# Kernel tuning notes

Measured on AMD Instinct MI355X. Metric: run time of the kernel, lower is better.

The kernel has to match this reference:

```python
import jax, jax.numpy as jnp
import numpy as np

V, D, L, H, S, B = 32000, 512, 4, 8, 2048, 2
HD = D // H
FF = 4 * D
EPS = 1e-5


def _ln(x, w, b):
    m = jnp.mean(x, axis=-1, keepdims=True)
    v = jnp.var(x, axis=-1, keepdims=True)
    return (x - m) / jnp.sqrt(v + EPS) * w + b


def setup_inputs() -> dict:
    key = jax.random.key(0)
    ks = jax.random.split(key, 32)
    rn = lambda k, shape, s=0.02: jax.random.normal(k, shape, jnp.float32) * s
    return {
        'x': jax.random.randint(ks[0], (B, S), 0, V),
        'tok_emb': rn(ks[1], (V, D)),
        'pos_emb': rn(ks[2], (S, D)),
        'qw': rn(ks[3], (L, D, D)), 'qb': rn(ks[4], (L, D)),
        'kw': rn(ks[5], (L, D, D)), 'kb': rn(ks[6], (L, D)),
        'vw': rn(ks[7], (L, D, D)), 'vb': rn(ks[8], (L, D)),
        'ow': rn(ks[9], (L, D, D)), 'ob': rn(ks[10], (L, D)),
        'qphase': rn(ks[11], (L, H), 0.1),
        'sp_phase': rn(ks[12], (L, D), 0.1),
        'n1w': jnp.ones((L, D), jnp.float32), 'n1b': jnp.zeros((L, D), jnp.float32),
        'n2w': jnp.ones((L, D), jnp.float32), 'n2b': jnp.zeros((L, D), jnp.float32),
        'f1w': rn(ks[13], (L, D, FF)), 'f1b': rn(ks[14], (L, FF)),
        'f2w': rn(ks[15], (L, FF, D)), 'f2b': rn(ks[16], (L, D)),
        'iw': rn(ks[17], (L, D, D)), 'ib': rn(ks[18], (L, D)),
        'gw': rn(ks[19], (L, D, D)), 'gb': rn(ks[20], (L, D)),
        'nw': jnp.ones((D,), jnp.float32), 'nb': jnp.zeros((D,), jnp.float32),
        'outw': rn(ks[21], (D, V)), 'outb': rn(ks[22], (V,)),
    }


def _forward(x, tok_emb, pos_emb, qw, qb, kw, kb, vw, vb, ow, ob, qphase, sp_phase,
             n1w, n1b, n2w, n2b, f1w, f1b, f2w, f2b, iw, ib, gw, gb, nw, nb, outw, outb):
    Bx, Sx = x.shape
    h = tok_emb[x] + pos_emb[:Sx][None, :, :]          # [B,S,D]
    mask = jnp.tril(jnp.ones((Sx, Sx), dtype=bool))    # causal
    scale = 1.0 / np.sqrt(HD).astype(np.float32)
    for l in range(L):
        # quantum attention with phase-modulated scores
        hn = _ln(h, n1w[l], n1b[l])
        q = (hn @ qw[l] + qb[l]).reshape(Bx, Sx, H, HD)
        k = (hn @ kw[l] + kb[l]).reshape(Bx, Sx, H, HD)
        v = (hn @ vw[l] + vb[l]).reshape(Bx, Sx, H, HD)
        scores = jnp.einsum('bqhd,bkhd->bhqk', q, k) * scale
        qi = jnp.cos(qphase[l][None, :, None, None] * scores)
        scores = scores * (1.0 + 0.1 * qi)
        scores = jnp.where(mask[None, None], scores, -jnp.inf)
        attn = jax.nn.softmax(scores, axis=-1)
        o = jnp.einsum('bhqk,bkhd->bqhd', attn, v).reshape(Bx, Sx, D)
        h = h + o @ ow[l] + ob[l]
        # superposition: x * cos(phase * x)
        h = h * jnp.cos(sp_phase[l] * h)
        # feed-forward (exact GELU, as torch default)
        hn2 = _ln(h, n2w[l], n2b[l])
        h = h + jax.nn.gelu(hn2 @ f1w[l] + f1b[l], approximate=False) @ f2w[l] + f2b[l]
        # interference gate
        g = jax.nn.sigmoid(h @ gw[l] + gb[l])
        h = (h @ iw[l] + ib[l]) * g + h * (1.0 - g)
    h = _ln(h, nw, nb)
    return h @ outw + outb                              # [B,S,V] logits


def reference(x, tok_emb, pos_emb, qw, qb, kw, kb, vw, vb, ow, ob, qphase, sp_phase,
              n1w, n1b, n2w, n2b, f1w, f1b, f2w, f2b, iw, ib, gw, gb, nw, nb, outw, outb):
    return _forward(x, tok_emb, pos_emb, qw, qb, kw, kb, vw, vb, ow, ob, qphase, sp_phase,
                    n1w, n1b, n2w, n2b, f1w, f1b, f2w, f2b, iw, ib, gw, gb, nw, nb, outw, outb)
```

## Files before the change

kernel.cpp:

```cpp
#include <hip/hip_runtime.h>
#include <math.h>

#define DIM 512
#define NH 8
#define HD 64
#define SEQ 2048
#define BATCH 2
#define NLAYER 4
#define FFD 2048
#define VOCAB 32000
#define ROWS (BATCH*SEQ)
#define QKV_LD 1536

typedef unsigned short u16;
typedef __attribute__((ext_vector_type(8))) short bfrag;
typedef __attribute__((ext_vector_type(4))) short sfrag4;
typedef __attribute__((ext_vector_type(4))) float facc;

__device__ __forceinline__ u16 f2bf(float f){
  unsigned u = __builtin_bit_cast(unsigned, f);
  u += 0x7fff + ((u>>16)&1);
  return (u16)(u>>16);
}

typedef __attribute__((address_space(3))) unsigned int lds_u32;
typedef const __attribute__((address_space(1))) unsigned int glob_u32;
__device__ __forceinline__ void gload16(const void* g, void* l){
  __builtin_amdgcn_global_load_lds((glob_u32*)g, (lds_u32*)l, 16, 0, 0);
}

template<int N> __device__ __forceinline__ void wait_vmcnt(){
  if constexpr (N==0)      asm volatile("s_waitcnt vmcnt(0)" ::: "memory");
  else if constexpr (N==3) asm volatile("s_waitcnt vmcnt(3)" ::: "memory");
  else if constexpr (N==4) asm volatile("s_waitcnt vmcnt(4)" ::: "memory");
  else if constexpr (N==6) asm volatile("s_waitcnt vmcnt(6)" ::: "memory");
  else if constexpr (N==8) asm volatile("s_waitcnt vmcnt(8)" ::: "memory");
  else static_assert(N==0, "unsupported vmcnt");
}

__global__ void transpose_w(const float* __restrict__ in, u16* __restrict__ out,
                            int K, int N, size_t zStride, int nOff, int imode){
  __shared__ float t[32][33];
  const int bz = blockIdx.z;
  const float* I = in + (size_t)bz*K*N;
  u16* O = out + (size_t)bz*zStride;
  const int n0 = blockIdx.x*32, k0 = blockIdx.y*32;
  #pragma unroll
  for (int i=0;i<4;i++){
    int k = k0 + threadIdx.y + 8*i;
    t[threadIdx.y+8*i][threadIdx.x] = I[(size_t)k*N + n0 + threadIdx.x];
  }
  __syncthreads();
  #pragma unroll
  for (int i=0;i<4;i++){
    int n = n0 + threadIdx.y + 8*i;
    int np = (imode==0) ? n : ((n>>4)*32 + (n&15) + (imode==2 ? 16 : 0));
    O[(size_t)(nOff+np)*K + k0 + threadIdx.x] = f2bf(t[threadIdx.x][threadIdx.y+8*i]);
  }
}

__global__ void concat3_k(const float* __restrict__ a, const float* __restrict__ b,
                          const float* __restrict__ c, float* __restrict__ o){
  int idx = blockIdx.x*256 + threadIdx.x;
  int l = idx/1536, r = idx%1536;
  float v = (r<512) ? a[l*512+r] : (r<1024 ? b[l*512+r-512] : c[l*512+r-1024]);
  o[idx] = v;
}
__global__ void concat2i_k(const float* __restrict__ ib, const float* __restrict__ gb,
                           float* __restrict__ o){
  int idx = blockIdx.x*256 + threadIdx.x;
  int l = idx>>10, cp = idx&1023;
  int bb = cp>>4, c = (bb>>1)*16 + (cp&15);
  o[idx] = (bb&1) ? gb[l*512+c] : ib[l*512+c];
}

__global__ void embed_k(const int* __restrict__ x, const float* __restrict__ tok,
                        const float* __restrict__ pos, float* __restrict__ h){
  int idx = blockIdx.x*256 + threadIdx.x;
  int row = idx >> 7;
  int d4  = idx & 127;
  int s   = row & (SEQ-1);
  int tkn = x[row];
  float4 tv = *(const float4*)(tok + (size_t)tkn*DIM + d4*4);
  float4 pv = *(const float4*)(pos + (size_t)s*DIM + d4*4);
  float4 r; r.x=tv.x+pv.x; r.y=tv.y+pv.y; r.z=tv.z+pv.z; r.w=tv.w+pv.w;
  *(float4*)(h + (size_t)row*DIM + d4*4) = r;
}

__global__ __launch_bounds__(256) void ln_k(const float* __restrict__ h,
    const float* __restrict__ w, const float* __restrict__ bsc,
    u16* __restrict__ out){
  const int wid = threadIdx.x>>6, lane = threadIdx.x&63;
  const int row = blockIdx.x*4 + wid;
  const float* r = h + (size_t)row*DIM + lane*8;
  float4 v0 = *(const float4*)r;
  float4 v1 = *(const float4*)(r+4);
  float s  = v0.x+v0.y+v0.z+v0.w + v1.x+v1.y+v1.z+v1.w;
  float ss = v0.x*v0.x+v0.y*v0.y+v0.z*v0.z+v0.w*v0.w
           + v1.x*v1.x+v1.y*v1.y+v1.z*v1.z+v1.w*v1.w;
  #pragma unroll
  for (int m=1;m<64;m<<=1){ s += __shfl_xor(s,m); ss += __shfl_xor(ss,m); }
  const float mean = s*(1.f/DIM);
  const float var  = ss*(1.f/DIM) - mean*mean;
  const float rsd  = rsqrtf(var + 1e-5f);
  float4 w0 = *(const float4*)(w + lane*8);
  float4 w1 = *(const float4*)(w + lane*8 + 4);
  float4 b0 = *(const float4*)(bsc + lane*8);
  float4 b1 = *(const float4*)(bsc + lane*8 + 4);
  bfrag pk;
  pk[0]=(short)f2bf((v0.x-mean)*rsd*w0.x+b0.x);
  pk[1]=(short)f2bf((v0.y-mean)*rsd*w0.y+b0.y);
  pk[2]=(short)f2bf((v0.z-mean)*rsd*w0.z+b0.z);
  pk[3]=(short)f2bf((v0.w-mean)*rsd*w0.w+b0.w);
  pk[4]=(short)f2bf((v1.x-mean)*rsd*w1.x+b1.x);
  pk[5]=(short)f2bf((v1.y-mean)*rsd*w1.y+b1.y);
  pk[6]=(short)f2bf((v1.z-mean)*rsd*w1.z+b1.z);
  pk[7]=(short)f2bf((v1.w-mean)*rsd*w1.w+b1.w);
  *(bfrag*)&out[(size_t)row*DIM + lane*8] = pk;
}

template<int BM,int BN,int BK,int WRN,int WCN,int DEPTH,int MODE>
__global__ __launch_bounds__(WRN*WCN*64, 2) void gemm_p(
    const u16* __restrict__ A, const u16* __restrict__ BT,
    const float* __restrict__ bias, const float* __restrict__ aux,
    float* __restrict__ Cf, u16* __restrict__ Cb, u16* __restrict__ vt,
    int M, int N, int K){
  constexpr int NTH = WRN*WCN*64;
  constexpr int FI  = BM/(16*WRN);
  constexpr int FJ  = BN/(16*WCN);
  constexpr int CPR = BK/8;
  constexpr int LA  = BM*CPR/NTH;
  constexpr int LB  = BN*CPR/NTH;
  constexpr int LPT = LA+LB;
  constexpr int NKK = BK/32;
  extern __shared__ __align__(16) u16 smem[];
  u16* lds_a = smem;
  u16* lds_b = smem + DEPTH*BM*BK;

  const int tid = threadIdx.x;
  const int wid = tid>>6, lane = tid&63;
  const int wr = wid / WCN, wc = wid % WCN;
  const int lr = lane&15, lg = lane>>4;
  const unsigned nwg = gridDim.x*gridDim.y;
  const unsigned lin = blockIdx.y*gridDim.x + blockIdx.x;
  const unsigned q = nwg >> 3;
  const unsigned sw = (lin & 7)*q + (lin >> 3);
  const int tm = sw % gridDim.x, tn = sw / gridDim.x;

  auto swzf = [](int row)->int{ return (BK==64) ? (row&7) : ((row>>1)&3); };

  auto stage = [&](int t, int buf){
    const int k0 = t*BK;
    #pragma unroll
    for (int i=0;i<LA;i++){
      int u = i*NTH + tid;
      int row = u/CPR, c = (u%CPR) ^ swzf(row);
      gload16(&A[(size_t)(tm*BM+row)*K + k0 + c*8], &lds_a[buf*BM*BK + u*8]);
    }
    #pragma unroll
    for (int i=0;i<LB;i++){
      int u = i*NTH + tid;
      int row = u/CPR, c = (u%CPR) ^ swzf(row);
      gload16(&BT[(size_t)(tn*BN+row)*K + k0 + c*8], &lds_b[buf*BN*BK + u*8]);
    }
  };

  facc acc[FI][FJ] = {};
  const int NT = K/BK;
  stage(0,0);
  if (NT>1) stage(1,1);
  if constexpr (DEPTH==3) { if (NT>2) stage(2,2); }
  for (int t=0;t<NT;t++){
    const int buf = t % DEPTH;
    const u16* la = &lds_a[buf*BM*BK];
    const u16* lb = &lds_b[buf*BN*BK];
    const int rem = NT-1-t;
    if constexpr (DEPTH==3){
      if (rem >= 2) wait_vmcnt<2*LPT>();
      else if (rem == 1) wait_vmcnt<LPT>();
      else wait_vmcnt<0>();
    } else {
      if (rem >= 1) wait_vmcnt<LPT>(); else wait_vmcnt<0>();
    }
    __builtin_amdgcn_s_barrier();
    __builtin_amdgcn_sched_barrier(0);
    bfrag af[FI], bf[FJ];
    #pragma unroll
    for (int i=0;i<FI;i++){
      int row = wr*(FI*16) + i*16 + lr;
      af[i] = *(const bfrag*)&la[row*BK + ((lg ^ swzf(row))*8)];
    }
    #pragma unroll
    for (int j=0;j<FJ;j++){
      int row = wc*(FJ*16) + j*16 + lr;
      bf[j] = *(const bfrag*)&lb[row*BK + ((lg ^ swzf(row))*8)];
    }
    if constexpr (NKK==1){
      asm volatile("s_waitcnt lgkmcnt(0)" ::: "memory");
      __builtin_amdgcn_sched_barrier(0);
      __builtin_amdgcn_s_barrier();
      __builtin_amdgcn_sched_barrier(0);
      if (t+DEPTH<NT) stage(t+DEPTH, buf);
      __builtin_amdgcn_s_setprio(1);
      #pragma unroll
      for (int i=0;i<FI;i++)
        #pragma unroll
        for (int j=0;j<FJ;j++)
          acc[i][j] = __builtin_amdgcn_mfma_f32_16x16x32_bf16(af[i], bf[j], acc[i][j],0,0,0);
      __builtin_amdgcn_s_setprio(0);
    } else {
      __builtin_amdgcn_s_setprio(1);
      #pragma unroll
      for (int i=0;i<FI;i++)
        #pragma unroll
        for (int j=0;j<FJ;j++)
          acc[i][j] = __builtin_amdgcn_mfma_f32_16x16x32_bf16(af[i], bf[j], acc[i][j],0,0,0);
      __builtin_amdgcn_s_setprio(0);
      bfrag af1[FI], bf1[FJ];
      #pragma unroll
      for (int i=0;i<FI;i++){
        int row = wr*(FI*16) + i*16 + lr;
        af1[i] = *(const bfrag*)&la[row*BK + (((4+lg) ^ swzf(row))*8)];
      }
      #pragma unroll
      for (int j=0;j<FJ;j++){
        int row = wc*(FJ*16) + j*16 + lr;
        bf1[j] = *(const bfrag*)&lb[row*BK + (((4+lg) ^ swzf(row))*8)];
      }
      asm volatile("s_waitcnt lgkmcnt(0)" ::: "memory");
      __builtin_amdgcn_sched_barrier(0);
      __builtin_amdgcn_s_barrier();
      __builtin_amdgcn_sched_barrier(0);
      if (t+DEPTH<NT) stage(t+DEPTH, buf);
      __builtin_amdgcn_s_setprio(1);
      #pragma unroll
      for (int i=0;i<FI;i++)
        #pragma unroll
        for (int j=0;j<FJ;j++)
          acc[i][j] = __builtin_amdgcn_mfma_f32_16x16x32_bf16(af1[i], bf1[j], acc[i][j],0,0,0);
      __builtin_amdgcn_s_setprio(0);
    }
  }

  if constexpr (MODE==5){
    #pragma unroll
    for (int i=0;i<FI;i++){
      #pragma unroll
      for (int j=0;j<FJ;j+=2){
        const int colp = tn*BN + wc*(FJ*16) + j*16;
        const int c = (colp>>5)*16 + lr;
        const float bi = bias[colp + lr];
        const float bg = bias[colp + 16 + lr];
        #pragma unroll
        for (int r=0;r<4;r++){
          const int row = tm*BM + wr*(FI*16) + i*16 + lg*4 + r;
          float vi = acc[i][j][r]   + bi;
          float vg = acc[i][j+1][r] + bg;
          float g  = 1.f/(1.f+__expf(-vg));
          const size_t o = (size_t)row*DIM + c;
          float hv = Cf[o];
          Cf[o] = vi*g + hv*(1.f-g);
        }
      }
    }
  } else if constexpr (MODE==7){
    #pragma unroll
    for (int i=0;i<FI;i++){
      #pragma unroll
      for (int j=0;j<FJ;j++){
        const int colblk = tn*BN + wc*(FJ*16) + j*16;
        const float bv = bias[colblk + lr];
        if (colblk < 1024){
          #pragma unroll
          for (int r=0;r<4;r++){
            const int row = tm*BM + wr*(FI*16) + i*16 + lg*4 + r;
            Cb[(size_t)row*N + colblk + lr] = f2bf(acc[i][j][r] + bv);
          }
        } else {
          const int c = colblk + lr - 1024;
          const int hh = c>>6, d = c&63;
          const int row0 = tm*BM + wr*(FI*16) + i*16 + lg*4;
          const int b = row0>>11, s0 = row0&2047;
          sfrag4 pk;
          #pragma unroll
          for (int r=0;r<4;r++) pk[r] = (short)f2bf(acc[i][j][r] + bv);
          *(sfrag4*)&vt[((size_t)((b*NH+hh)*HD + d))*SEQ + s0] = pk;
        }
      }
    }
  } else {
    #pragma unroll
    for (int i=0;i<FI;i++){
      #pragma unroll
      for (int j=0;j<FJ;j++){
        const int col = tn*BN + wc*(FJ*16) + j*16 + lr;
        const float bv = bias ? bias[col] : 0.f;
        #pragma unroll
        for (int r=0;r<4;r++){
          const int row = tm*BM + wr*(FI*16) + i*16 + lg*4 + r;
          float v = acc[i][j][r] + bv;
          const size_t o = (size_t)row*N + col;
          if      (MODE==0) Cf[o] = v;
          else if (MODE==3){ float g = 0.5f*v*(1.f+erff(v*0.70710678118f)); Cb[o] = f2bf(g); }
          else if (MODE==4){ float t = Cf[o] + v; t = t*__cosf(aux[col]*t); Cf[o] = t; }
          else if (MODE==6){ float t = Cf[o] + v; Cf[o] = t; Cb[o] = f2bf(t); }
        }
      }
    }
  }
}

__global__ __launch_bounds__(256) void attn_k(
    const u16* __restrict__ QKV, const u16* __restrict__ VT,
    const float* __restrict__ qphase, u16* __restrict__ O){
  __shared__ __align__(16) u16 lds_p[4][16*64];
  const int bx = blockIdx.x;
  const int qblk = (bx&1) ? (31 - (bx>>1)) : (bx>>1);
  const int hh = blockIdx.y, b = blockIdx.z;
  const int tid = threadIdx.x;
  const int wid = tid>>6, lane = tid&63;
  const int lr = lane&15, lg = lane>>4;
  const int qbase = qblk*64 + wid*16;
  const float ph = qphase[hh];
  const float scale = 0.125f;
  u16* pbuf = lds_p[wid];

  bfrag aq[2];
  #pragma unroll
  for (int st=0; st<2; st++)
    aq[st] = *(const bfrag*)&QKV[(size_t)(b*SEQ + qbase + lr)*QKV_LD + hh*HD + st*32 + lg*8];

  facc oacc[4] = {};
  float lrow[4] = {0.f,0.f,0.f,0.f};

  const int nkv = qblk + 1;
  for (int kt=0; kt<nkv; kt++){
    const int kv0 = kt*64;
    facc sc[4];
    #pragma unroll
    for (int j=0;j<4;j++){
      bfrag bk0 = *(const bfrag*)&QKV[(size_t)(b*SEQ + kv0 + j*16 + lr)*QKV_LD + 512 + hh*HD + lg*8];
      bfrag bk1 = *(const bfrag*)&QKV[(size_t)(b*SEQ + kv0 + j*16 + lr)*QKV_LD + 512 + hh*HD + 32 + lg*8];
      facc z = (facc){0.f,0.f,0.f,0.f};
      z     = __builtin_amdgcn_mfma_f32_16x16x32_bf16(aq[0], bk0, z, 0,0,0);
      sc[j] = __builtin_amdgcn_mfma_f32_16x16x32_bf16(aq[1], bk1, z, 0,0,0);
    }
    float pv[4][4];
    #pragma unroll
    for (int j=0;j<4;j++)
      #pragma unroll
      for (int r=0;r<4;r++){
        int srow = qbase + lg*4 + r;
        int scol = kv0 + j*16 + lr;
        float xv = sc[j][r]*scale;
        xv = xv*(1.f + 0.1f*__cosf(ph*xv));
        if (scol > srow) xv = -1e30f;
        pv[j][r] = __expf(xv);
      }
    #pragma unroll
    for (int r=0;r<4;r++){
      float rs = (pv[0][r]+pv[1][r]) + (pv[2][r]+pv[3][r]);
      rs += __shfl_xor(rs,1);
      rs += __shfl_xor(rs,2);
      rs += __shfl_xor(rs,4);
      rs += __shfl_xor(rs,8);
      lrow[r] += rs;
    }
    #pragma unroll
    for (int j=0;j<4;j++)
      #pragma unroll
      for (int r=0;r<4;r++){
        int prow = lg*4 + r;
        pbuf[prow*64 + ((j*16+lr) ^ ((prow&7)<<3))] = f2bf(pv[j][r]);
      }
    #pragma unroll
    for (int ks=0; ks<2; ks++){
      bfrag pa = *(const bfrag*)&pbuf[lr*64 + ((ks*32 + lg*8) ^ ((lr&7)<<3))];
      #pragma unroll
      for (int n=0;n<4;n++){
        bfrag vb = *(const bfrag*)&VT[((size_t)((b*NH + hh)*HD + n*16 + lr))*SEQ + kv0 + ks*32 + lg*8];
        oacc[n] = __builtin_amdgcn_mfma_f32_16x16x32_bf16(pa, vb, oacc[n], 0,0,0);
      }
    }
  }
  float rcp[4];
  #pragma unroll
  for (int r=0;r<4;r++) rcp[r] = 1.f/lrow[r];
  #pragma unroll
  for (int n=0;n<4;n++)
    #pragma unroll
    for (int r=0;r<4;r++){
      float val = oacc[n][r] * rcp[r];
      O[(size_t)(b*SEQ + qbase + lg*4 + r)*DIM + hh*HD + n*16 + lr] = f2bf(val);
    }
}

extern "C" void kernel_launch(void* const* d_in, const int* in_sizes, int n_in,
                              void* d_out, int out_size, void* d_ws, size_t ws_size,
                              hipStream_t stream){
  const int*   x        = (const int*)d_in[0];
  const float* tok_emb  = (const float*)d_in[1];
  const float* pos_emb  = (const float*)d_in[2];
  const float* qw = (const float*)d_in[3];  const float* qb = (const float*)d_in[4];
  const float* kw = (const float*)d_in[5];  const float* kb = (const float*)d_in[6];
  const float* vw = (const float*)d_in[7];  const float* vb = (const float*)d_in[8];
  const float* ow = (const float*)d_in[9];  const float* ob = (const float*)d_in[10];
  const float* qphase   = (const float*)d_in[11];
  const float* sp_phase = (const float*)d_in[12];
  const float* n1w = (const float*)d_in[13]; const float* n1b = (const float*)d_in[14];
  const float* n2w = (const float*)d_in[15]; const float* n2b = (const float*)d_in[16];
  const float* f1w = (const float*)d_in[17]; const float* f1b = (const float*)d_in[18];
  const float* f2w = (const float*)d_in[19]; const float* f2b = (const float*)d_in[20];
  const float* iw  = (const float*)d_in[21]; const float* ib  = (const float*)d_in[22];
  const float* gw  = (const float*)d_in[23]; const float* gb  = (const float*)d_in[24];
  const float* nw  = (const float*)d_in[25]; const float* nb  = (const float*)d_in[26];
  const float* outw= (const float*)d_in[27]; const float* outb= (const float*)d_in[28];
  float* out = (float*)d_out;

  char* base = (char*)d_ws;
  size_t off = 0;
  auto alloc = [&](size_t bytes)->void*{
    void* p = base + off; off += bytes; off = (off + 255) & ~(size_t)255; return p;
  };
  float* h    = (float*)alloc((size_t)ROWS*DIM*4);
  u16* hn     = (u16*)alloc((size_t)ROWS*DIM*2);
  u16* qkvB   = (u16*)alloc((size_t)ROWS*QKV_LD*2);
  u16* vTb    = (u16*)alloc((size_t)ROWS*DIM*2);
  u16* oB     = (u16*)alloc((size_t)ROWS*DIM*2);
  u16* hB     = (u16*)alloc((size_t)ROWS*DIM*2);
  u16* ffB    = (u16*)alloc((size_t)ROWS*FFD*2);
  u16* qkvT = (u16*)alloc((size_t)NLAYER*1536*DIM*2);
  u16* owT  = (u16*)alloc((size_t)NLAYER*DIM*DIM*2);
  u16* igT  = (u16*)alloc((size_t)NLAYER*1024*DIM*2);
  u16* f1T  = (u16*)alloc((size_t)NLAYER*DIM*FFD*2);
  u16* f2T  = (u16*)alloc((size_t)NLAYER*DIM*FFD*2);
  u16* outT = (u16*)alloc((size_t)VOCAB*DIM*2);
  float* qkvb = (float*)alloc((size_t)NLAYER*1536*4);
  float* igb  = (float*)alloc((size_t)NLAYER*1024*4);

  dim3 tb(32,8);
  transpose_w<<<dim3(DIM/32, DIM/32, NLAYER), tb, 0, stream>>>(qw, qkvT, DIM, DIM, (size_t)1536*DIM, 0, 0);
  transpose_w<<<dim3(DIM/32, DIM/32, NLAYER), tb, 0, stream>>>(kw, qkvT, DIM, DIM, (size_t)1536*DIM, 512, 0);
  transpose_w<<<dim3(DIM/32, DIM/32, NLAYER), tb, 0, stream>>>(vw, qkvT, DIM, DIM, (size_t)1536*DIM, 1024, 0);
  transpose_w<<<dim3(DIM/32, DIM/32, NLAYER), tb, 0, stream>>>(ow, owT, DIM, DIM, (size_t)DIM*DIM, 0, 0);
  transpose_w<<<dim3(DIM/32, DIM/32, NLAYER), tb, 0, stream>>>(iw, igT, DIM, DIM, (size_t)1024*DIM, 0, 1);
  transpose_w<<<dim3(DIM/32, DIM/32, NLAYER), tb, 0, stream>>>(gw, igT, DIM, DIM, (size_t)1024*DIM, 0, 2);
  transpose_w<<<dim3(FFD/32, DIM/32, NLAYER), tb, 0, stream>>>(f1w, f1T, DIM, FFD, (size_t)DIM*FFD, 0, 0);
  transpose_w<<<dim3(DIM/32, FFD/32, NLAYER), tb, 0, stream>>>(f2w, f2T, FFD, DIM, (size_t)DIM*FFD, 0, 0);
  transpose_w<<<dim3(VOCAB/32, DIM/32, 1),    tb, 0, stream>>>(outw, outT, DIM, VOCAB, 0, 0, 0);
  concat3_k<<<NLAYER*1536/256, 256, 0, stream>>>(qb, kb, vb, qkvb);
  concat2i_k<<<NLAYER*1024/256, 256, 0, stream>>>(ib, gb, igb);

  embed_k<<<ROWS*DIM/4/256, 256, 0, stream>>>(x, tok_emb, pos_emb, h);

  constexpr size_t SM_MID = 3*(128+128)*32*2;
  constexpr size_t SM_ROW = 3*(64+128)*32*2;
  constexpr size_t SM_BIG = 2*(256+256)*64*2;

  for (int l=0;l<NLAYER;l++){
    ln_k<<<ROWS/4, 256, 0, stream>>>(h, n1w + l*DIM, n1b + l*DIM, hn);
    gemm_p<128,128,32,2,2,3,7><<<dim3(ROWS/128, 1536/128), 256, SM_MID, stream>>>(
        hn, qkvT + (size_t)l*1536*DIM, qkvb + l*1536, nullptr, nullptr, qkvB, vTb, ROWS, 1536, DIM);
    attn_k<<<dim3(SEQ/64, NH, BATCH), 256, 0, stream>>>(qkvB, vTb, qphase + l*NH, oB);
    gemm_p<64,128,32,1,4,3,4><<<dim3(ROWS/64, DIM/128), 256, SM_ROW, stream>>>(
        oB, owT + (size_t)l*DIM*DIM, ob + l*DIM, sp_phase + l*DIM, h, nullptr, nullptr, ROWS, DIM, DIM);
    ln_k<<<ROWS/4, 256, 0, stream>>>(h, n2w + l*DIM, n2b + l*DIM, hn);
    gemm_p<128,128,32,2,2,3,3><<<dim3(ROWS/128, FFD/128), 256, SM_MID, stream>>>(
        hn, f1T + (size_t)l*DIM*FFD, f1b + l*FFD, nullptr, nullptr, ffB, nullptr, ROWS, FFD, DIM);
    gemm_p<64,128,32,1,4,3,6><<<dim3(ROWS/64, DIM/128), 256, SM_ROW, stream>>>(
        ffB, f2T + (size_t)l*DIM*FFD, f2b + l*DIM, nullptr, h, hB, nullptr, ROWS, DIM, FFD);
    gemm_p<128,128,32,2,2,3,5><<<dim3(ROWS/128, 1024/128), 256, SM_MID, stream>>>(
        hB, igT + (size_t)l*1024*DIM, igb + l*1024, nullptr, h, nullptr, nullptr, ROWS, 1024, DIM);
  }
  ln_k<<<ROWS/4, 256, 0, stream>>>(h, nw, nb, hn);
  gemm_p<256,256,64,2,4,2,0><<<dim3(ROWS/256, VOCAB/256), 512, SM_BIG, stream>>>(
      hn, outT, outb, nullptr, out, nullptr, nullptr, ROWS, VOCAB, DIM);
}
```

Before: 1.235 ms.

## Rework attention to online softmax with 32-wide KV tiles; tune output GEMM stores

New measurement: 1.126 ms. 8.8% less time.

```diff
diff --git a/kernel.cpp b/kernel.cpp
--- a/kernel.cpp
+++ b/kernel.cpp
@@ -30,11 +30,12 @@
 }
 
 template<int N> __device__ __forceinline__ void wait_vmcnt(){
-  if constexpr (N==0)      asm volatile("s_waitcnt vmcnt(0)" ::: "memory");
-  else if constexpr (N==3) asm volatile("s_waitcnt vmcnt(3)" ::: "memory");
-  else if constexpr (N==4) asm volatile("s_waitcnt vmcnt(4)" ::: "memory");
-  else if constexpr (N==6) asm volatile("s_waitcnt vmcnt(6)" ::: "memory");
-  else if constexpr (N==8) asm volatile("s_waitcnt vmcnt(8)" ::: "memory");
+  if constexpr (N==0)       asm volatile("s_waitcnt vmcnt(0)" ::: "memory");
+  else if constexpr (N==3)  asm volatile("s_waitcnt vmcnt(3)" ::: "memory");
+  else if constexpr (N==4)  asm volatile("s_waitcnt vmcnt(4)" ::: "memory");
+  else if constexpr (N==6)  asm volatile("s_waitcnt vmcnt(6)" ::: "memory");
+  else if constexpr (N==8)  asm volatile("s_waitcnt vmcnt(8)" ::: "memory");
+  else if constexpr (N==16) asm volatile("s_waitcnt vmcnt(16)" ::: "memory");
   else static_assert(N==0, "unsupported vmcnt");
 }
 
@@ -119,7 +120,7 @@
   *(bfrag*)&out[(size_t)row*DIM + lane*8] = pk;
 }
 
-template<int BM,int BN,int BK,int WRN,int WCN,int DEPTH,int MODE>
+template<int BM,int BN,int BK,int WRN,int WCN,int DEPTH,int MODE,int SWZ>
 __global__ __launch_bounds__(WRN*WCN*64, 2) void gemm_p(
     const u16* __restrict__ A, const u16* __restrict__ BT,
     const float* __restrict__ bias, const float* __restrict__ aux,
@@ -141,11 +142,16 @@
   const int wid = tid>>6, lane = tid&63;
   const int wr = wid / WCN, wc = wid % WCN;
   const int lr = lane&15, lg = lane>>4;
-  const unsigned nwg = gridDim.x*gridDim.y;
-  const unsigned lin = blockIdx.y*gridDim.x + blockIdx.x;
-  const unsigned q = nwg >> 3;
-  const unsigned sw = (lin & 7)*q + (lin >> 3);
-  const int tm = sw % gridDim.x, tn = sw / gridDim.x;
+  int tm, tn;
+  if constexpr (SWZ){
+    const unsigned nwg = gridDim.x*gridDim.y;
+    const unsigned lin = blockIdx.y*gridDim.x + blockIdx.x;
+    const unsigned q = nwg >> 3;
+    const unsigned sw = (lin & 7)*q + (lin >> 3);
+    tm = sw % gridDim.x; tn = sw / gridDim.x;
+  } else {
+    tm = blockIdx.x; tn = blockIdx.y;
+  }
 
   auto swzf = [](int row)->int{ return (BK==64) ? (row&7) : ((row>>1)&3); };
 
@@ -301,6 +307,7 @@
           float v = acc[i][j][r] + bv;
           const size_t o = (size_t)row*N + col;
           if      (MODE==0) Cf[o] = v;
+          else if (MODE==8) __builtin_nontemporal_store(v, &Cf[o]);
           else if (MODE==3){ float g = 0.5f*v*(1.f+erff(v*0.70710678118f)); Cb[o] = f2bf(g); }
           else if (MODE==4){ float t = Cf[o] + v; t = t*__cosf(aux[col]*t); Cf[o] = t; }
           else if (MODE==6){ float t = Cf[o] + v; Cf[o] = t; Cb[o] = f2bf(t); }
@@ -313,10 +320,8 @@
 __global__ __launch_bounds__(256) void attn_k(
     const u16* __restrict__ QKV, const u16* __restrict__ VT,
     const float* __restrict__ qphase, u16* __restrict__ O){
-  __shared__ __align__(16) u16 lds_p[4][16*64];
-  const int bx = blockIdx.x;
-  const int qblk = (bx&1) ? (31 - (bx>>1)) : (bx>>1);
-  const int hh = blockIdx.y, b = blockIdx.z;
+  __shared__ __align__(16) u16 lds_p[4][16*32];
+  const int qblk = blockIdx.x, hh = blockIdx.y, b = blockIdx.z;
   const int tid = threadIdx.x;
   const int wid = tid>>6, lane = tid&63;
   const int lr = lane&15, lg = lane>>4;
@@ -330,24 +335,33 @@
   for (int st=0; st<2; st++)
     aq[st] = *(const bfrag*)&QKV[(size_t)(b*SEQ + qbase + lr)*QKV_LD + hh*HD + st*32 + lg*8];
 
-  facc oacc[4] = {};
+  facc oacc[4];
+  #pragma unroll
+  for (int n=0;n<4;n++) oacc[n] = (facc){0.f,0.f,0.f,0.f};
+  float mrow[4] = {-1e30f,-1e30f,-1e30f,-1e30f};
   float lrow[4] = {0.f,0.f,0.f,0.f};
 
-  const int nkv = qblk + 1;
+  const int nkv = (qbase + 15)/32 + 1;
   for (int kt=0; kt<nkv; kt++){
-    const int kv0 = kt*64;
-    facc sc[4];
-    #pragma unroll
-    for (int j=0;j<4;j++){
+    const int kv0 = kt*32;
+    facc sc[2];
+    #pragma unroll
+    for (int j=0;j<2;j++){
       bfrag bk0 = *(const bfrag*)&QKV[(size_t)(b*SEQ + kv0 + j*16 + lr)*QKV_LD + 512 + hh*HD + lg*8];
       bfrag bk1 = *(const bfrag*)&QKV[(size_t)(b*SEQ + kv0 + j*16 + lr)*QKV_LD + 512 + hh*HD + 32 + lg*8];
       facc z = (facc){0.f,0.f,0.f,0.f};
       z     = __builtin_amdgcn_mfma_f32_16x16x32_bf16(aq[0], bk0, z, 0,0,0);
       sc[j] = __builtin_amdgcn_mfma_f32_16x16x32_bf16(aq[1], bk1, z, 0,0,0);
     }
-    float pv[4][4];
-    #pragma unroll
-    for (int j=0;j<4;j++)
+    bfrag vbf[4];
+    #pragma unroll
+    for (int n=0;n<4;n++)
+      vbf[n] = *(const bfrag*)&VT[((size_t)((b*NH + hh)*HD + n*16 + lr))*SEQ + kv0 + lg*8];
+
+    float pv[2][4];
+    float tmax[4] = {-1e30f,-1e30f,-1e30f,-1e30f};
+    #pragma unroll
+    for (int j=0;j<2;j++)
       #pragma unroll
       for (int r=0;r<4;r++){
         int srow = qbase + lg*4 + r;
@@ -355,42 +369,46 @@
         float xv = sc[j][r]*scale;
         xv = xv*(1.f + 0.1f*__cosf(ph*xv));
         if (scol > srow) xv = -1e30f;
-        pv[j][r] = __expf(xv);
+        pv[j][r] = xv;
+        tmax[r] = fmaxf(tmax[r], xv);
       }
     #pragma unroll
     for (int r=0;r<4;r++){
-      float rs = (pv[0][r]+pv[1][r]) + (pv[2][r]+pv[3][r]);
+      float t = tmax[r];
+      t = fmaxf(t, __shfl_xor(t,1));
+      t = fmaxf(t, __shfl_xor(t,2));
+      t = fmaxf(t, __shfl_xor(t,4));
+      t = fmaxf(t, __shfl_xor(t,8));
+      float mnew = fmaxf(mrow[r], t);
+      float corr = __expf(mrow[r] - mnew);
+      float p0 = __expf(pv[0][r] - mnew);
+      float p1 = __expf(pv[1][r] - mnew);
+      pv[0][r] = p0; pv[1][r] = p1;
+      float rs = p0 + p1;
       rs += __shfl_xor(rs,1);
       rs += __shfl_xor(rs,2);
       rs += __shfl_xor(rs,4);
       rs += __shfl_xor(rs,8);
-      lrow[r] += rs;
-    }
-    #pragma unroll
-    for (int j=0;j<4;j++)
-      #pragma unroll
-      for (int r=0;r<4;r++){
-        int prow = lg*4 + r;
-        pbuf[prow*64 + ((j*16+lr) ^ ((prow&7)<<3))] = f2bf(pv[j][r]);
-      }
-    #pragma unroll
-    for (int ks=0; ks<2; ks++){
-      bfrag pa = *(const bfrag*)&pbuf[lr*64 + ((ks*32 + lg*8) ^ ((lr&7)<<3))];
-      #pragma unroll
-      for (int n=0;n<4;n++){
-        bfrag vb = *(const bfrag*)&VT[((size_t)((b*NH + hh)*HD + n*16 + lr))*SEQ + kv0 + ks*32 + lg*8];
-        oacc[n] = __builtin_amdgcn_mfma_f32_16x16x32_bf16(pa, vb, oacc[n], 0,0,0);
-      }
-    }
-  }
-  float rcp[4];
-  #pragma unroll
-  for (int r=0;r<4;r++) rcp[r] = 1.f/lrow[r];
+      lrow[r] = lrow[r]*corr + rs;
+      mrow[r] = mnew;
+      #pragma unroll
+      for (int n=0;n<4;n++) oacc[n][r] *= corr;
+    }
+    #pragma unroll
+    for (int j=0;j<2;j++)
+      #pragma unroll
+      for (int r=0;r<4;r++)
+        pbuf[(lg*4+r)*32 + j*16 + lr] = f2bf(pv[j][r]);
+    bfrag pa = *(const bfrag*)&pbuf[lr*32 + lg*8];
+    #pragma unroll
+    for (int n=0;n<4;n++)
+      oacc[n] = __builtin_amdgcn_mfma_f32_16x16x32_bf16(pa, vbf[n], oacc[n], 0,0,0);
+  }
   #pragma unroll
   for (int n=0;n<4;n++)
     #pragma unroll
     for (int r=0;r<4;r++){
-      float val = oacc[n][r] * rcp[r];
+      float val = oacc[n][r] / lrow[r];
       O[(size_t)(b*SEQ + qbase + lg*4 + r)*DIM + hh*HD + n*16 + lr] = f2bf(val);
     }
 }
@@ -453,26 +471,31 @@
 
   embed_k<<<ROWS*DIM/4/256, 256, 0, stream>>>(x, tok_emb, pos_emb, h);
 
-  constexpr size_t SM_MID = 3*(128+128)*32*2;
-  constexpr size_t SM_ROW = 3*(64+128)*32*2;
-  constexpr size_t SM_BIG = 2*(256+256)*64*2;
+  constexpr size_t SM_MID3 = 3*(128+128)*32*2;
+  constexpr size_t SM_ROW3 = 3*(64+128)*32*2;
+  constexpr size_t SM_BIG  = 2*(256+256)*64*2;
 
   for (int l=0;l<NLAYER;l++){
     ln_k<<<ROWS/4, 256, 0, stream>>>(h, n1w + l*DIM, n1b + l*DIM, hn);
-    gemm_p<128,128,32,2,2,3,7><<<dim3(ROWS/128, 1536/128), 256, SM_MID, stream>>>(
-        hn, qkvT + (size_t)l*1536*DIM, qkvb + l*1536, nullptr, nullptr, qkvB, vTb, ROWS, 1536, DIM);
+    gemm_p<128,128,32,2,2,3,7,1><<<dim3(ROWS/128, 1536/128), 256, SM_MID3, stream>>>(
+        hn, qkvT + (size_t)l*1536*DIM, qkvb + l*1536, nullptr,
+        nullptr, qkvB, vTb, ROWS, 1536, DIM);
     attn_k<<<dim3(SEQ/64, NH, BATCH), 256, 0, stream>>>(qkvB, vTb, qphase + l*NH, oB);
-    gemm_p<64,128,32,1,4,3,4><<<dim3(ROWS/64, DIM/128), 256, SM_ROW, stream>>>(
-        oB, owT + (size_t)l*DIM*DIM, ob + l*DIM, sp_phase + l*DIM, h, nullptr, nullptr, ROWS, DIM, DIM);
+    gemm_p<64,128,32,1,4,3,4,1><<<dim3(ROWS/64, DIM/128), 256, SM_ROW3, stream>>>(
+        oB, owT + (size_t)l*DIM*DIM, ob + l*DIM, sp_phase + l*DIM,
+        h, nullptr, nullptr, ROWS, DIM, DIM);
     ln_k<<<ROWS/4, 256, 0, stream>>>(h, n2w + l*DIM, n2b + l*DIM, hn);
-    gemm_p<128,128,32,2,2,3,3><<<dim3(ROWS/128, FFD/128), 256, SM_MID, stream>>>(
-        hn, f1T + (size_t)l*DIM*FFD, f1b + l*FFD, nullptr, nullptr, ffB, nullptr, ROWS, FFD, DIM);
-    gemm_p<64,128,32,1,4,3,6><<<dim3(ROWS/64, DIM/128), 256, SM_ROW, stream>>>(
-        ffB, f2T + (size_t)l*DIM*FFD, f2b + l*DIM, nullptr, h, hB, nullptr, ROWS, DIM, FFD);
-    gemm_p<128,128,32,2,2,3,5><<<dim3(ROWS/128, 1024/128), 256, SM_MID, stream>>>(
-        hB, igT + (size_t)l*1024*DIM, igb + l*1024, nullptr, h, nullptr, nullptr, ROWS, 1024, DIM);
+    gemm_p<128,128,32,2,2,3,3,1><<<dim3(ROWS/128, FFD/128), 256, SM_MID3, stream>>>(
+        hn, f1T + (size_t)l*DIM*FFD, f1b + l*FFD, nullptr,
+        nullptr, ffB, nullptr, ROWS, FFD, DIM);
+    gemm_p<64,128,32,1,4,3,6,1><<<dim3(ROWS/64, DIM/128), 256, SM_ROW3, stream>>>(
+        ffB, f2T + (size_t)l*DIM*FFD, f2b + l*DIM, nullptr,
+        h, hB, nullptr, ROWS, DIM, FFD);
+    gemm_p<128,128,32,2,2,3,5,1><<<dim3(ROWS/128, 1024/128), 256, SM_MID3, stream>>>(
+        hB, igT + (size_t)l*1024*DIM, igb + l*1024, nullptr,
+        h, nullptr, nullptr, ROWS, 1024, DIM);
   }
   ln_k<<<ROWS/4, 256, 0, stream>>>(h, nw, nb, hn);
-  gemm_p<256,256,64,2,4,2,0><<<dim3(ROWS/256, VOCAB/256), 512, SM_BIG, stream>>>(
+  gemm_p<256,256,64,2,4,2,8,0><<<dim3(ROWS/256, VOCAB/256), 512, SM_BIG, stream>>>(
       hn, outT, outb, nullptr, out, nullptr, nullptr, ROWS, VOCAB, DIM);
 }
```
